# Kernel optimization log

Hardware: AMD Instinct MI355X
Metric: run time of the kernel (lower is better)

The kernel has to match this reference:

```python
import jax, jax.numpy as jnp
import numpy as np

EPS = 1e-10


def setup_inputs() -> dict:
    key = jax.random.key(0)
    k1, k2 = jax.random.split(key)
    supports = jax.random.normal(k1, (32, 512, 1024), dtype=jnp.float32)
    targets = jax.random.normal(k2, (32, 512, 1024), dtype=jnp.float32)
    return {"supports": supports, "targets": targets}


def reference(supports, targets):
    # targets: [B, T, D], supports: [B, S, D] -> sim: [B, T, S]
    # F.cosine_similarity(a, b, eps): dot / max(||a||*||b||, eps)
    dots = jnp.einsum("btd,bsd->bts", targets, supports)
    t_norm = jnp.linalg.norm(targets, axis=-1)   # [B, T]
    s_norm = jnp.linalg.norm(supports, axis=-1)  # [B, S]
    denom = jnp.maximum(t_norm[:, :, None] * s_norm[:, None, :], EPS)
    sim = dots / denom
    # normalize=True default: map (-1, 1) -> (0, 1)
    return (sim + 1.0) * 0.5
```

## Files before the change

kernel.cpp:

```cpp
#include <hip/hip_runtime.h>
#include <hip/hip_bf16.h>

typedef __attribute__((ext_vector_type(4))) float f32x4;

#define NBATCH 32
#define NT 512
#define NS 512
#define ND 1024
#define BM 128
#define BN 256
#define BK 32
#define NK (ND / BK)
#define ROWB 32

__device__ __forceinline__ int cvtpk4(float a, float b, float c, float d) {
    int v = __builtin_amdgcn_cvt_pk_fp8_f32(a, b, 0, false);
    v = __builtin_amdgcn_cvt_pk_fp8_f32(c, d, v, true);
    return v;
}

__device__ __forceinline__ int2 cvt8(float4 a, float4 b) {
    return make_int2(cvtpk4(a.x, a.y, a.z, a.w), cvtpk4(b.x, b.y, b.z, b.w));
}

__device__ __forceinline__ float ssq4(float s, float4 a) {
    return fmaf(a.x, a.x, fmaf(a.y, a.y, fmaf(a.z, a.z, fmaf(a.w, a.w, s))));
}

__global__ __launch_bounds__(1024, 4)
void paircos_mfma(const float* __restrict__ sup, const float* __restrict__ tgt,
                  float* __restrict__ out) {
    __shared__ __align__(16) unsigned char As[2][BM * ROWB];
    __shared__ __align__(16) unsigned char Bs[2][BN * ROWB];
    __shared__ float tn[BM];
    __shared__ float sn[BN];

    const int tid = threadIdx.x;
    const int l    = blockIdx.x;
    const int wgid = (l & 7) * 32 + (l >> 3);
    const int b    = wgid >> 3;
    const int til  = wgid & 7;
    const int bt0  = (til >> 1) * BM;
    const int bs0  = (til & 1) * BN;

    const int seg  = tid & 3;
    const int srow = tid >> 2;
    const bool stA = (tid < 512);

    const float* gB = sup + (size_t)b * NS * ND + (size_t)(bs0 + srow) * ND + seg * 8;
    const float* gA = tgt + (size_t)b * NT * ND + (size_t)(bt0 + srow) * ND + seg * 8;

    const int wave = tid >> 6;
    const int lane = tid & 63;
    const int wr  = (wave >> 3) * 64;
    const int wc  = (wave & 7) * 32;
    const int lhi = lane >> 4;
    const int llo = lane & 15;

    f32x4 acc[4][2];
#pragma unroll
    for (int m = 0; m < 4; ++m)
#pragma unroll
        for (int n = 0; n < 2; ++n)
            acc[m][n] = (f32x4){0.f, 0.f, 0.f, 0.f};

    float sqa = 0.f, sqb = 0.f;

    float4 pA0, pA1, pB0, pB1;

    const int offw = srow * ROWB + (((seg + (srow >> 2)) & 3) * 8);

#define LOADT(KK)                                                              \
    do {                                                                       \
        pB0 = *reinterpret_cast<const float4*>(gB + (KK) * BK);                \
        pB1 = *reinterpret_cast<const float4*>(gB + (KK) * BK + 4);            \
        if (stA) {                                                             \
            pA0 = *reinterpret_cast<const float4*>(gA + (KK) * BK);            \
            pA1 = *reinterpret_cast<const float4*>(gA + (KK) * BK + 4);        \
        }                                                                      \
    } while (0)

#define STORET(P)                                                              \
    do {                                                                       \
        sqb = ssq4(ssq4(sqb, pB0), pB1);                                       \
        *reinterpret_cast<int2*>(&Bs[P][offw]) = cvt8(pB0, pB1);               \
        if (stA) {                                                             \
            sqa = ssq4(ssq4(sqa, pA0), pA1);                                   \
            *reinterpret_cast<int2*>(&As[P][offw]) = cvt8(pA0, pA1);           \
        }                                                                      \
    } while (0)

#define FRAG_READ(P)                                                           \
    do {                                                                       \
        _Pragma("unroll") for (int m = 0; m < 4; ++m) {                        \
            const int row = wr + m * 16 + llo;                                 \
            const int off = row * ROWB + (((lhi + (row >> 2)) & 3) * 8);       \
            af[m] = *reinterpret_cast<const long*>(&As[P][off]);               \
        }                                                                      \
        _Pragma("unroll") for (int n = 0; n < 2; ++n) {                        \
            const int row = wc + n * 16 + llo;                                 \
            const int off = row * ROWB + (((lhi + (row >> 2)) & 3) * 8);       \
            bfr[n] = *reinterpret_cast<const long*>(&Bs[P][off]);              \
        }                                                                      \
    } while (0)

#define MFMA_BLOCK()                                                           \
    do {                                                                       \
        __builtin_amdgcn_s_setprio(1);                                         \
        _Pragma("unroll") for (int m = 0; m < 4; ++m)                          \
            _Pragma("unroll") for (int n = 0; n < 2; ++n)                      \
                acc[m][n] = __builtin_amdgcn_mfma_f32_16x16x32_fp8_fp8(        \
                    af[m], bfr[n], acc[m][n], 0, 0, 0);                        \
        __builtin_amdgcn_s_setprio(0);                                         \
    } while (0)

#define PHASE_FENCE()                                                          \
    do {                                                                       \
        asm volatile("s_waitcnt lgkmcnt(0)" ::: "memory");                     \
        __builtin_amdgcn_s_barrier();                                          \
        asm volatile("" ::: "memory");                                         \
    } while (0)

    LOADT(0);
    STORET(0);
    LOADT(1);
    PHASE_FENCE();

    for (int k = 0; k < NK; ++k) {
        const int cur = k & 1;
        long af[4], bfr[2];
        FRAG_READ(cur);
        if (k + 1 < NK) STORET(cur ^ 1);
        if (k + 2 < NK) LOADT(k + 2);
        MFMA_BLOCK();
        PHASE_FENCE();
    }

    sqb += __shfl_xor(sqb, 1);
    sqb += __shfl_xor(sqb, 2);
    if (seg == 0) sn[srow] = sqrtf(sqb);
    if (stA) {
        sqa += __shfl_xor(sqa, 1);
        sqa += __shfl_xor(sqa, 2);
        if (seg == 0) tn[srow] = sqrtf(sqa);
    }
    __syncthreads();

    float* outp = out + (size_t)b * NT * NS;
#pragma unroll
    for (int m = 0; m < 4; ++m) {
        const int lr0 = wr + m * 16 + lhi * 4;
#pragma unroll
        for (int n = 0; n < 2; ++n) {
            const int lc = wc + n * 16 + llo;
            const float snv = sn[lc];
            const int col = bs0 + lc;
#pragma unroll
            for (int j = 0; j < 4; ++j) {
                const float denom = fmaxf(tn[lr0 + j] * snv, 1e-10f);
                outp[(size_t)(bt0 + lr0 + j) * NS + col] =
                    acc[m][n][j] / denom * 0.5f + 0.5f;
            }
        }
    }
}

extern "C" void kernel_launch(void* const* d_in, const int* in_sizes, int n_in,
                              void* d_out, int out_size, void* d_ws, size_t ws_size,
                              hipStream_t stream) {
    const float* sup = (const float*)d_in[0];
    const float* tgt = (const float*)d_in[1];
    float* out = (float*)d_out;
    (void)in_sizes; (void)n_in; (void)out_size; (void)d_ws; (void)ws_size;
    paircos_mfma<<<dim3(32 * 8), 1024, 0, stream>>>(sup, tgt, out);
}
```

Before: 32.83 us.

## Enlarge output tile to 256x256 and balance global loads across all threads

Doubles the target-side tile so each workgroup computes a 256x256 block, with every wave owning a 64x64 sub-tile and half as many workgroups launched. All 1024 threads now load and convert 16 floats each, instead of B threads carrying twice the load. The LDS swizzle is switched to an XOR pattern. This cuts redundant global reads of the inputs and raises MFMA work per fragment load, at the cost of launching only 128 workgroups, which leaves many CUs idle.

```diff
diff --git a/kernel.cpp b/kernel.cpp
--- a/kernel.cpp
+++ b/kernel.cpp
@@ -7,7 +7,7 @@
 #define NT 512
 #define NS 512
 #define ND 1024
-#define BM 128
+#define BM 256
 #define BN 256
 #define BK 32
 #define NK (ND / BK)
@@ -17,10 +17,6 @@
     int v = __builtin_amdgcn_cvt_pk_fp8_f32(a, b, 0, false);
     v = __builtin_amdgcn_cvt_pk_fp8_f32(c, d, v, true);
     return v;
-}
-
-__device__ __forceinline__ int2 cvt8(float4 a, float4 b) {
-    return make_int2(cvtpk4(a.x, a.y, a.z, a.w), cvtpk4(b.x, b.y, b.z, b.w));
 }
 
 __device__ __forceinline__ float ssq4(float s, float4 a) {
@@ -37,69 +33,72 @@
 
     const int tid = threadIdx.x;
     const int l    = blockIdx.x;
-    const int wgid = (l & 7) * 32 + (l >> 3);
-    const int b    = wgid >> 3;
-    const int til  = wgid & 7;
+    const int wgid = (l & 7) * 16 + (l >> 3);
+    const int b    = wgid >> 2;
+    const int til  = wgid & 3;
     const int bt0  = (til >> 1) * BM;
     const int bs0  = (til & 1) * BN;
 
-    const int seg  = tid & 3;
-    const int srow = tid >> 2;
-    const bool stA = (tid < 512);
+    const bool isA = (tid < 512);
+    const int  sr  = (tid & 511) >> 1;
+    const int  sh  = tid & 1;
 
-    const float* gB = sup + (size_t)b * NS * ND + (size_t)(bs0 + srow) * ND + seg * 8;
-    const float* gA = tgt + (size_t)b * NT * ND + (size_t)(bt0 + srow) * ND + seg * 8;
+    const float* gsrc = (isA ? tgt + (size_t)b * NT * ND + (size_t)(bt0 + sr) * ND
+                             : sup + (size_t)b * NS * ND + (size_t)(bs0 + sr) * ND)
+                        + sh * 16;
 
     const int wave = tid >> 6;
     const int lane = tid & 63;
-    const int wr  = (wave >> 3) * 64;
-    const int wc  = (wave & 7) * 32;
+    const int wr  = (wave >> 2) * 64;
+    const int wc  = (wave & 3) * 64;
     const int lhi = lane >> 4;
     const int llo = lane & 15;
 
-    f32x4 acc[4][2];
+    f32x4 acc[4][4];
 #pragma unroll
     for (int m = 0; m < 4; ++m)
 #pragma unroll
-        for (int n = 0; n < 2; ++n)
+        for (int n = 0; n < 4; ++n)
             acc[m][n] = (f32x4){0.f, 0.f, 0.f, 0.f};
 
-    float sqa = 0.f, sqb = 0.f;
+    float sq = 0.f;
 
-    float4 pA0, pA1, pB0, pB1;
+    float4 p0, p1, p2, p3;
 
-    const int offw = srow * ROWB + (((seg + (srow >> 2)) & 3) * 8);
+    const int offw = sr * ROWB + ((2 * sh) ^ ((sr >> 1) & 2)) * 8;
+    unsigned char* const dst0 = (isA ? &As[0][0] : &Bs[0][0]) + offw;
+    unsigned char* const dst1 = (isA ? &As[1][0] : &Bs[1][0]) + offw;
 
 #define LOADT(KK)                                                              \
     do {                                                                       \
-        pB0 = *reinterpret_cast<const float4*>(gB + (KK) * BK);                \
-        pB1 = *reinterpret_cast<const float4*>(gB + (KK) * BK + 4);            \
-        if (stA) {                                                             \
-            pA0 = *reinterpret_cast<const float4*>(gA + (KK) * BK);            \
-            pA1 = *reinterpret_cast<const float4*>(gA + (KK) * BK + 4);        \
-        }                                                                      \
+        const float* s_ = gsrc + (KK) * BK;                                    \
+        p0 = *reinterpret_cast<const float4*>(s_);                             \
+        p1 = *reinterpret_cast<const float4*>(s_ + 4);                         \
+        p2 = *reinterpret_cast<const float4*>(s_ + 8);                         \
+        p3 = *reinterpret_cast<const float4*>(s_ + 12);                        \
     } while (0)
 
 #define STORET(P)                                                              \
     do {                                                                       \
-        sqb = ssq4(ssq4(sqb, pB0), pB1);                                       \
-        *reinterpret_cast<int2*>(&Bs[P][offw]) = cvt8(pB0, pB1);               \
-        if (stA) {                                                             \
-            sqa = ssq4(ssq4(sqa, pA0), pA1);                                   \
-            *reinterpret_cast<int2*>(&As[P][offw]) = cvt8(pA0, pA1);           \
-        }                                                                      \
+        sq = ssq4(ssq4(ssq4(ssq4(sq, p0), p1), p2), p3);                       \
+        int4 v_;                                                               \
+        v_.x = cvtpk4(p0.x, p0.y, p0.z, p0.w);                                 \
+        v_.y = cvtpk4(p1.x, p1.y, p1.z, p1.w);                                 \
+        v_.z = cvtpk4(p2.x, p2.y, p2.z, p2.w);                                 \
+        v_.w = cvtpk4(p3.x, p3.y, p3.z, p3.w);                                 \
+        *reinterpret_cast<int4*>((P) ? dst1 : dst0) = v_;                      \
     } while (0)
 
 #define FRAG_READ(P)                                                           \
     do {                                                                       \
         _Pragma("unroll") for (int m = 0; m < 4; ++m) {                        \
             const int row = wr + m * 16 + llo;                                 \
-            const int off = row * ROWB + (((lhi + (row >> 2)) & 3) * 8);       \
+            const int off = row * ROWB + ((lhi ^ ((row >> 1) & 2)) * 8);       \
             af[m] = *reinterpret_cast<const long*>(&As[P][off]);               \
         }                                                                      \
-        _Pragma("unroll") for (int n = 0; n < 2; ++n) {                        \
+        _Pragma("unroll") for (int n = 0; n < 4; ++n) {                        \
             const int row = wc + n * 16 + llo;                                 \
-            const int off = row * ROWB + (((lhi + (row >> 2)) & 3) * 8);       \
+            const int off = row * ROWB + ((lhi ^ ((row >> 1) & 2)) * 8);       \
             bfr[n] = *reinterpret_cast<const long*>(&Bs[P][off]);              \
         }                                                                      \
     } while (0)
@@ -108,7 +107,7 @@
     do {                                                                       \
         __builtin_amdgcn_s_setprio(1);                                         \
         _Pragma("unroll") for (int m = 0; m < 4; ++m)                          \
-            _Pragma("unroll") for (int n = 0; n < 2; ++n)                      \
+            _Pragma("unroll") for (int n = 0; n < 4; ++n)                      \
                 acc[m][n] = __builtin_amdgcn_mfma_f32_16x16x32_fp8_fp8(        \
                     af[m], bfr[n], acc[m][n], 0, 0, 0);                        \
         __builtin_amdgcn_s_setprio(0);                                         \
@@ -128,7 +127,7 @@
 
     for (int k = 0; k < NK; ++k) {
         const int cur = k & 1;
-        long af[4], bfr[2];
+        long af[4], bfr[4];
         FRAG_READ(cur);
         if (k + 1 < NK) STORET(cur ^ 1);
         if (k + 2 < NK) LOADT(k + 2);
@@ -136,13 +135,10 @@
         PHASE_FENCE();
     }
 
-    sqb += __shfl_xor(sqb, 1);
-    sqb += __shfl_xor(sqb, 2);
-    if (seg == 0) sn[srow] = sqrtf(sqb);
-    if (stA) {
-        sqa += __shfl_xor(sqa, 1);
-        sqa += __shfl_xor(sqa, 2);
-        if (seg == 0) tn[srow] = sqrtf(sqa);
+    sq += __shfl_xor(sq, 1);
+    if (sh == 0) {
+        if (isA) tn[sr] = sqrtf(sq);
+        else     sn[sr] = sqrtf(sq);
     }
     __syncthreads();
 
@@ -151,7 +147,7 @@
     for (int m = 0; m < 4; ++m) {
         const int lr0 = wr + m * 16 + lhi * 4;
 #pragma unroll
-        for (int n = 0; n < 2; ++n) {
+        for (int n = 0; n < 4; ++n) {
             const int lc = wc + n * 16 + llo;
             const float snv = sn[lc];
             const int col = bs0 + lc;
@@ -172,5 +168,5 @@
     const float* tgt = (const float*)d_in[1];
     float* out = (float*)d_out;
     (void)in_sizes; (void)n_in; (void)out_size; (void)d_ws; (void)ws_size;
-    paircos_mfma<<<dim3(32 * 8), 1024, 0, stream>>>(sup, tgt, out);
+    paircos_mfma<<<dim3(32 * 4), 1024, 0, stream>>>(sup, tgt, out);
 }
```

Measured after the change: 52.16 us. +58.9%, slower.
